# Kernel optimization log

Hardware: AMD Instinct MI355X
Metric: run time of the kernel (lower is better)

## Reference

```python
import jax, jax.numpy as jnp
import numpy as np

B, S, IN_DIM, LATENT, SYM = 16, 256, 512, 512, 128
NUM_NODES, NUM_CODES, MAX_OPS, MAX_BUS = 4, 512, 4, 32
HALT_EPS, MAX_SEQ = 1e-3, 256


def setup_inputs() -> dict:
    key = jax.random.key(0)
    ks = jax.random.split(key, 10)

    def lin(k, out_d, in_d, pre=()):
        kw, kb = jax.random.split(k)
        lim = 1.0 / np.sqrt(in_d).astype(np.float32)
        w = jax.random.uniform(kw, pre + (out_d, in_d), minval=-lim, maxval=lim, dtype=jnp.float32)
        b = jax.random.uniform(kb, pre + (out_d,), minval=-lim, maxval=lim, dtype=jnp.float32)
        return w, b

    x = jax.random.normal(ks[0], (B, S, IN_DIM), jnp.float32)
    ipw, ipb = lin(ks[1], LATENT, IN_DIM)
    tp = jax.random.normal(ks[2], (1, MAX_SEQ, LATENT), jnp.float32)
    N = (NUM_NODES,)
    sw, sb = lin(ks[3], SYM, LATENT, N)
    qw, qb = lin(ks[4], 1, SYM, N)
    rw, rb = lin(ks[5], LATENT, 2 * LATENT, N)
    c1w, c1b = lin(ks[6], LATENT, LATENT + SYM, N)
    c2w, c2b = lin(ks[7], LATENT, LATENT, N)
    cb = jax.random.normal(ks[8], (NUM_NODES, NUM_CODES, SYM), jnp.float32)
    return {"x": x, "input_proj_w": ipw, "input_proj_b": ipb, "token_prompts": tp,
            "sym_w": sw, "sym_b": sb, "qry_w": qw, "qry_b": qb,
            "read_w": rw, "read_b": rb, "c1_w": c1w, "c1_b": c1b,
            "c2_w": c2w, "c2_b": c2b, "codebook": cb}


def _forward(x, input_proj_w, input_proj_b, token_prompts, sym_w, sym_b, qry_w, qry_b,
             read_w, read_b, c1_w, c1_b, c2_w, c2_b, codebook):
    Bx, Sx, _ = x.shape
    N = Bx * Sx
    # input projection + positional prompts
    out = jnp.einsum('bsi,li->bsl', x, input_proj_w) + input_proj_b + token_prompts[:, :Sx, :]
    prev_out = out
    active = jnp.ones((Bx, Sx), bool)
    token_tags = jnp.zeros((Bx, Sx, SYM), x.dtype)
    # TensorBus rolling buffers ([max_bus, B, S, dim]); with default cfg the roll branch never fires
    sym_buf = jnp.zeros((MAX_BUS, Bx, Sx, SYM), x.dtype)          # slot 0 = zero tags (initial append)
    out_buf = jnp.zeros((MAX_BUS, Bx, Sx, LATENT), x.dtype).at[0].set(out)
    msg_mask = jnp.zeros((MAX_BUS,), bool).at[0].set(True)
    ptr = 1  # static python int: appends are a fixed unrolled schedule (1 + MAX_OPS*NUM_NODES <= MAX_BUS)
    slot_ids = jnp.arange(MAX_BUS)

    for t in range(MAX_OPS):
        # snapshot of active messages for this op step (get_active)
        snap_active = msg_mask & (slot_ids < ptr)                  # [MAX_BUS]
        syms_flat = sym_buf.reshape(MAX_BUS, N, SYM)
        outs_flat = out_buf.reshape(MAX_BUS, N, LATENT)
        keep_all = jnp.ones((MAX_BUS,), bool)
        for n in range(NUM_NODES):
            # relevance of each bus message per token; inactive slots masked out of argmax
            rel = jnp.einsum('tnd,d->tn', syms_flat, qry_w[n, 0]) + qry_b[n, 0]
            rel = jnp.where(snap_active[:, None], rel, jnp.asarray(-1e9, rel.dtype))
            top = jnp.argmax(rel, axis=0)                          # [N] chosen message per token
            chosen = jnp.take_along_axis(outs_flat, top[None, :, None], axis=0)[0]  # [N, LATENT]
            bus_ctx = chosen.reshape(Bx, Sx, LATENT)
            z = jnp.concatenate([out, bus_ctx], axis=-1)
            z_read = jnp.einsum('bsk,lk->bsl', z, read_w[n]) + read_b[n]
            raw_sym = jnp.einsum('bsl,dl->bsd', z_read, sym_w[n]) + sym_b[n]
            # EMA quantizer (eval): nearest codebook entry by euclidean distance
            flat = raw_sym.reshape(-1, SYM)
            cbn = codebook[n]
            d2 = (jnp.sum(flat * flat, axis=-1, keepdims=True)
                  - 2.0 * flat @ cbn.T + jnp.sum(cbn * cbn, axis=-1))
            idx = jnp.argmin(d2, axis=-1)
            quant = cbn[idx].reshape(Bx, Sx, SYM)
            h = jnp.concatenate([z_read, quant], axis=-1)
            hid = jax.nn.relu(jnp.einsum('bsk,lk->bsl', h, c1_w[n]) + c1_b[n])
            node_out = jnp.einsum('bsl,ol->bso', hid, c2_w[n]) + c2_b[n] + out
            # halting / selective update
            delta = jnp.linalg.norm(node_out - prev_out, axis=-1)
            halt = (delta < HALT_EPS) & active
            assigned = active if t > 0 else jnp.ones_like(active)
            upd = assigned & jnp.logical_not(halt)
            out = jnp.where(upd[..., None], node_out, out)
            token_tags = jnp.where(upd[..., None], quant, token_tags)
            # bus.append
            sym_buf = sym_buf.at[ptr].set(quant)
            out_buf = out_buf.at[ptr].set(node_out)
            msg_mask = msg_mask.at[ptr].set(True)
            ptr += 1
            # keep_mask: messages never selected by any token stay alive
            counts = jnp.zeros((MAX_BUS,), jnp.int32).at[top].add(1)
            keep_all = keep_all & (counts == 0)
            active = active & jnp.logical_not(halt)
            prev_out = out
        # mark_consumed: ones over valid slots ANDed with per-node keep masks at snapshot-active
        # slots (inactive/new slots get True -> faithful to the torch init_global_mask quirk)
        msg_mask = (slot_ids < ptr) & keep_all
    return out


def reference(x, input_proj_w, input_proj_b, token_prompts, sym_w, sym_b, qry_w, qry_b,
              read_w, read_b, c1_w, c1_b, c2_w, c2_b, codebook):
    return _forward(x, input_proj_w, input_proj_b, token_prompts, sym_w, sym_b, qry_w, qry_b,
                    read_w, read_b, c1_w, c1_b, c2_w, c2_b, codebook)
```

## Files before the change

kernel.cpp:

```cpp
#include <hip/hip_runtime.h>
#include <math.h>

namespace {

typedef _Float16 f16;
typedef __attribute__((ext_vector_type(8))) _Float16 f16x8;
typedef __attribute__((ext_vector_type(4))) float f32x4;

constexpr int TOK = 4096;
constexpr int DL  = 512;
constexpr int DS  = 128;
constexpr int NC  = 512;
constexpr int NSLOT = 13;

__device__ __forceinline__ float wsum(float v){
  #pragma unroll
  for(int o=32;o>0;o>>=1) v += __shfl_xor(v,o);
  return v;
}

__device__ __forceinline__ void gload16(const void* g, void* l){
  __builtin_amdgcn_global_load_lds(
      (const __attribute__((address_space(1))) unsigned int*)g,
      (__attribute__((address_space(3))) unsigned int*)l, 16, 0, 0);
}

__device__ __forceinline__ int slotb(int row, int g){
  return (((row ^ ((row>>2)&1))<<2) | (g ^ (row&3))) << 4;
}

template<int AMODE,int EPI>
__global__ __launch_bounds__(256,2) void mgemm(
    const f16* __restrict__ A1h, const f16* __restrict__ A1l,
    const f16* __restrict__ A2h, const f16* __restrict__ A2l,
    const int* __restrict__ gidx,
    const f16* __restrict__ Bh, const f16* __restrict__ Bl,
    const float* __restrict__ bias, const float* __restrict__ res,
    float* __restrict__ Cf, f16* __restrict__ Ch, f16* __restrict__ Cl,
    f16* __restrict__ C2h, f16* __restrict__ C2l,
    float* __restrict__ scpv, int* __restrict__ scpi, int* __restrict__ idxg,
    int K, int K0)
{
  constexpr int SMB = 16384;
  __shared__ __align__(16) char smem[3*SMB];
  __shared__ int gsel[64];
  __shared__ float redv[4][32];
  __shared__ int   redi[4][32];
  const int tid = threadIdx.x, w = tid>>6, l = tid&63;
  const int m0 = blockIdx.x*64, n0 = blockIdx.y*64;
  const int NK = K>>5, SW = K0>>5;

  if(AMODE==2){
    if(tid<64){
      int m = m0+tid;
      float bv = -INFINITY; int bi = 0;
      #pragma unroll
      for(int y=0;y<8;y++){
        float v = scpv[(size_t)y*TOK + m];
        if(v > bv){ bv=v; bi=scpi[(size_t)y*TOK + m]; }
      }
      gsel[tid]=bi;
      idxg[m]=bi;
    }
    __syncthreads();
  }

  const f16* sp[4]; const f16* sp2[4]; int loff[4];
  #pragma unroll
  for(int i=0;i<4;i++){
    int c = 4*w+i;
    int isA = (c<8);
    int plane = isA ? (c>>2) : ((c-8)>>2);
    int cidx  = isA ? (c&3)  : ((c-8)&3);
    loff[i] = (isA?0:8192) + plane*4096 + cidx*1024;
    int s = (cidx<<6) + l;
    int rp = s>>2, row = rp ^ ((rp>>2)&1), g = (s&3) ^ (row&3);
    int g8 = g<<3;
    if(isA){
      int m = m0 + row;
      const f16* p1 = (plane? A1l : A1h) + ((size_t)m<<9) + g8;
      sp[i] = p1;
      if(AMODE==1)      sp2[i] = (plane? A2l : A2h) + ((size_t)gidx[m]<<21) + ((size_t)m<<9) + g8;
      else if(AMODE==2) sp2[i] = (plane? A2l : A2h) + ((size_t)gsel[row]<<7) + g8;
      else              sp2[i] = p1;
    } else {
      sp[i] = (plane? Bl : Bh) + (size_t)(n0+row)*K + g8;
      sp2[i] = sp[i];
    }
  }

  const int wr = w>>1, wc = w&1, q = l>>4, r = l&15;
  int aoff[2], boff[2];
  #pragma unroll
  for(int i=0;i<2;i++) aoff[i] = slotb(32*wr + 16*i + r, q);
  #pragma unroll
  for(int j=0;j<2;j++) boff[j] = 8192 + slotb(32*wc + 16*j + r, q);

  f32x4 acc1[2][2] = {}, acc2[2][2] = {};

  auto advance = [&](int snext){
    #pragma unroll
    for(int i=0;i<4;i++){
      if(AMODE!=0 && (4*w+i)<8 && snext==SW) sp[i] = sp2[i];
      else                                    sp[i] += 32;
    }
  };

  #pragma unroll
  for(int i=0;i<4;i++) gload16(sp[i], smem + loff[i]);
  advance(1);
  #pragma unroll
  for(int i=0;i<4;i++) gload16(sp[i], smem + SMB + loff[i]);
  advance(2);
  asm volatile("s_waitcnt vmcnt(4)" ::: "memory");
  __builtin_amdgcn_s_barrier();

  int roff = 0, soff = 2*SMB;
  for(int kt=0; kt<NK; ++kt){
    const char* Lb = smem + roff;
    f16x8 ah[2], al[2], bh[2], bl[2];
    #pragma unroll
    for(int i=0;i<2;i++){
      ah[i] = *(const f16x8*)(Lb + aoff[i]);
      al[i] = *(const f16x8*)(Lb + 4096 + aoff[i]);
    }
    #pragma unroll
    for(int j=0;j<2;j++){
      bh[j] = *(const f16x8*)(Lb + boff[j]);
      bl[j] = *(const f16x8*)(Lb + 4096 + boff[j]);
    }
    if(kt+2 < NK){
      #pragma unroll
      for(int i=0;i<4;i++) gload16(sp[i], smem + soff + loff[i]);
      advance(kt+3);
    }
    #pragma unroll
    for(int i=0;i<2;i++)
      #pragma unroll
      for(int j=0;j<2;j++){
        acc1[i][j] = __builtin_amdgcn_mfma_f32_16x16x32_f16(ah[i], bh[j], acc1[i][j], 0,0,0);
        acc2[i][j] = __builtin_amdgcn_mfma_f32_16x16x32_f16(ah[i], bl[j], acc2[i][j], 0,0,0);
        acc2[i][j] = __builtin_amdgcn_mfma_f32_16x16x32_f16(al[i], bh[j], acc2[i][j], 0,0,0);
      }
    if(kt+2 < NK){
      asm volatile("s_waitcnt vmcnt(4)" ::: "memory");
      __builtin_amdgcn_s_barrier();
    } else if(kt+1 < NK){
      asm volatile("s_waitcnt vmcnt(0)" ::: "memory");
      __builtin_amdgcn_s_barrier();
    }
    roff = (roff==2*SMB)? 0 : roff+SMB;
    soff = (soff==2*SMB)? 0 : soff+SMB;
  }

  if(EPI!=1){
    #pragma unroll
    for(int i=0;i<2;i++)
      #pragma unroll
      for(int j=0;j<2;j++)
        #pragma unroll
        for(int rr=0;rr<4;rr++){
          int rowm = m0 + 32*wr + 16*i + 4*q + rr;
          int coln = n0 + 32*wc + 16*j + r;
          size_t o = ((size_t)rowm<<9) + coln;
          float v = acc1[i][j][rr] + acc2[i][j][rr]*(1.0f/2048.0f) + bias[coln];
          if(EPI==2) v = fmaxf(v, 0.f);
          if(EPI==3) v += res[o];
          if(EPI==4) v += res[(((size_t)(rowm&255))<<9) + coln];
          if(EPI==3 || EPI==4) Cf[o] = v;
          if(EPI==0 || EPI==2 || EPI==4){
            f16 h = (f16)v;
            Ch[o] = h; Cl[o] = (f16)((v-(float)h)*2048.0f);
          }
          if(EPI==4){
            f16 h = (f16)v;
            C2h[o] = h; C2l[o] = (f16)((v-(float)h)*2048.0f);
          }
        }
  } else {
    #pragma unroll
    for(int i=0;i<2;i++)
      #pragma unroll
      for(int rr=0;rr<4;rr++){
        float v0 = acc1[i][0][rr] + acc2[i][0][rr]*(1.0f/2048.0f) + bias[n0+32*wc+r];
        float v1 = acc1[i][1][rr] + acc2[i][1][rr]*(1.0f/2048.0f) + bias[n0+32*wc+16+r];
        float bv; int bc;
        if(v1 > v0){ bv=v1; bc=n0+32*wc+16+r; } else { bv=v0; bc=n0+32*wc+r; }
        #pragma unroll
        for(int o=1;o<16;o<<=1){
          float ov = __shfl_xor(bv,o); int oi = __shfl_xor(bc,o);
          if(ov>bv || (ov==bv && oi<bc)){ bv=ov; bc=oi; }
        }
        if(r==0){ redv[w][16*i+4*q+rr]=bv; redi[w][16*i+4*q+rr]=bc; }
      }
    __syncthreads();
    if(tid<64){
      int wr2 = tid>>5, li = tid&31;
      float bv = redv[2*wr2][li]; int bc = redi[2*wr2][li];
      float ov = redv[2*wr2+1][li]; int oi = redi[2*wr2+1][li];
      if(ov>bv || (ov==bv && oi<bc)){ bv=ov; bc=oi; }
      scpv[(size_t)blockIdx.y*TOK + m0 + tid] = bv;
      scpi[(size_t)blockIdx.y*TOK + m0 + tid] = bc;
    }
  }
}

__global__ void split_k(const float* __restrict__ src, f16* __restrict__ hi,
                        f16* __restrict__ lo, int n){
  for(int i = blockIdx.x*256 + threadIdx.x; i < n; i += gridDim.x*256){
    float v = src[i];
    f16 h = (f16)v;
    hi[i] = h;
    lo[i] = (f16)((v - (float)h)*2048.0f);
  }
}

__global__ __launch_bounds__(256)
void wcomb_k(const float* __restrict__ A, const float* __restrict__ Wall,
             float* __restrict__ C)
{
  constexpr int T=256;
  __shared__ float As[32][68];
  __shared__ float Ws[32][132];
  const int tid = threadIdx.x;
  const int m0 = blockIdx.x*64, n0 = blockIdx.y*128;
  const float* W = Wall + (size_t)(m0>>9)*DS*DL;
  const int ty = tid>>4, tx = tid&15;
  float4 pa[2], pw[4];
  auto loadA = [&](int k0){
    #pragma unroll
    for(int it=0; it<2; ++it){
      int v = tid + T*it; int rr = v>>3, c4 = v&7;
      pa[it] = *(const float4*)(A + (size_t)(m0+rr)*DS + k0 + (c4<<2));
    }
  };
  auto loadW = [&](int k0){
    #pragma unroll
    for(int it=0; it<4; ++it){
      int v = tid + T*it; int rr = v>>5, c4 = v&31;
      pw[it] = *(const float4*)(W + (size_t)(k0+rr)*DL + n0 + (c4<<2));
    }
  };
  float acc[4][8];
  #pragma unroll
  for(int i=0;i<4;i++)
    #pragma unroll
    for(int j=0;j<8;j++) acc[i][j]=0.f;
  loadA(0); loadW(0);
  for(int k0=0; k0<DS; k0+=32){
    __syncthreads();
    #pragma unroll
    for(int it=0; it<2; ++it){
      int v = tid + T*it; int rr=v>>3, c4=v&7;
      As[(c4<<2)+0][rr]=pa[it].x; As[(c4<<2)+1][rr]=pa[it].y;
      As[(c4<<2)+2][rr]=pa[it].z; As[(c4<<2)+3][rr]=pa[it].w;
    }
    #pragma unroll
    for(int it=0; it<4; ++it){
      int v = tid + T*it; int rr=v>>5, c4=v&31;
      *(float4*)&Ws[rr][c4<<2] = pw[it];
    }
    __syncthreads();
    if(k0+32 < DS){ loadA(k0+32); loadW(k0+32); }
    #pragma unroll
    for(int kk=0; kk<32; kk++){
      float4 a4 = *(const float4*)&As[kk][ty<<2];
      float4 b0 = *(const float4*)&Ws[kk][tx<<2];
      float4 b1 = *(const float4*)&Ws[kk][64+(tx<<2)];
      float a[4]={a4.x,a4.y,a4.z,a4.w};
      float b[8]={b0.x,b0.y,b0.z,b0.w,b1.x,b1.y,b1.z,b1.w};
      #pragma unroll
      for(int i=0;i<4;i++)
        #pragma unroll
        for(int j=0;j<8;j++) acc[i][j] = fmaf(a[i], b[j], acc[i][j]);
    }
  }
  #pragma unroll
  for(int i=0;i<4;i++){
    int m = m0 + (ty<<2) + i;
    #pragma unroll
    for(int j=0;j<8;j++){
      int n = n0 + ((j<4)? (tx<<2)+j : 64+(tx<<2)+(j-4));
      C[((size_t)m<<9)+n] = acc[i][j];
    }
  }
}

__global__ void init_k(int* __restrict__ msg, int* __restrict__ act,
                       float* __restrict__ relc, const float* __restrict__ qb,
                       int* __restrict__ cons){
  int i = blockIdx.x*256 + threadIdx.x;
  if(i < TOK){
    act[i] = 1;
    #pragma unroll
    for(int nn=0;nn<4;nn++) relc[nn*TOK + i] = qb[nn];
  }
  if(i < 32){ msg[i] = (i==0) ? 1 : 0; cons[i] = 0; }
}

__global__ void bias2_k(const float* __restrict__ cb, const float* __restrict__ sb,
                        float* __restrict__ b2){
  int row = blockIdx.x*4 + (threadIdx.x>>6);
  int lane = threadIdx.x&63;
  const float* cv = cb + ((size_t)row<<7);
  const float* sbn = sb + ((row>>9)<<7);
  float c0=cv[lane], c1=cv[lane+64];
  float nrm = c0*c0 + c1*c1;
  float dt  = c0*sbn[lane] + c1*sbn[lane+64];
  nrm = wsum(nrm); dt = wsum(dt);
  if(lane==0) b2[row] = dt - 0.5f*nrm;
}

__global__ void relmax_k(const float* __restrict__ relc, const int* __restrict__ msg,
                         int pt, int node, int* __restrict__ top, int* __restrict__ cons){
  int tok = blockIdx.x*256 + threadIdx.x;
  float best = -1e9f; int bs = 0;
  for(int s=0;s<pt;s++){
    float v = msg[s] ? relc[(size_t)((s<<2)+node)*TOK + tok] : -1e9f;
    if(v > best){ best = v; bs = s; }
  }
  top[tok] = bs;
  cons[bs] = 1;
}

__global__ void mupdate_k(const float* __restrict__ no_, float* __restrict__ out,
                          f16* __restrict__ outh, f16* __restrict__ outl,
                          f16* __restrict__ slabh, f16* __restrict__ slabl,
                          float* __restrict__ relc, const int* __restrict__ idx,
                          const float* __restrict__ cbn, const float* __restrict__ qw,
                          const float* __restrict__ qb, int* __restrict__ act,
                          int* __restrict__ cons, int* __restrict__ msg,
                          int t, int ptr, int pe){
  int m = blockIdx.x*4 + (threadIdx.x>>6);
  int lane = threadIdx.x&63;
  const float* nrow = no_ + ((size_t)m<<9);
  float* orow = out + ((size_t)m<<9);
  float nv[8]; float s=0.f;
  #pragma unroll
  for(int rr=0;rr<8;rr++){
    int c = lane + (rr<<6);
    nv[rr]=nrow[c];
    float d = nv[rr]-orow[c]; s += d*d;
  }
  s = wsum(s);
  float delta = sqrtf(s);
  int a = act[m];
  int halt = (delta < 1e-3f) && a;
  int assigned = (t>0) ? a : 1;
  int upd = assigned && !halt;
  if(lane==0) act[m] = a && !halt;
  if(upd){
    #pragma unroll
    for(int rr=0;rr<8;rr++){
      int c = lane + (rr<<6);
      float v = nv[rr];
      orow[c] = v;
      f16 h = (f16)v;
      outh[((size_t)m<<9)+c] = h;
      outl[((size_t)m<<9)+c] = (f16)((v-(float)h)*2048.0f);
    }
  }
  if(ptr >= 0){
    size_t so = (((size_t)ptr)<<21) + ((size_t)m<<9);
    #pragma unroll
    for(int rr=0;rr<8;rr++){
      int c = lane + (rr<<6);
      float v = nv[rr];
      f16 h = (f16)v;
      slabh[so+c] = h;
      slabl[so+c] = (f16)((v-(float)h)*2048.0f);
    }
    const float* qv = cbn + ((size_t)idx[m]<<7);
    float q0=qv[lane], q1=qv[lane+64];
    #pragma unroll
    for(int nn=0;nn<4;nn++){
      float pr = q0*qw[(nn<<7)+lane] + q1*qw[(nn<<7)+64+lane];
      pr = wsum(pr);
      if(lane==0) relc[(size_t)((ptr<<2)+nn)*TOK + m] = pr + qb[nn];
    }
  }
  if(pe >= 0 && blockIdx.x==0 && threadIdx.x < 32){
    int s2 = threadIdx.x;
    msg[s2] = (s2 < pe) && !cons[s2];
    cons[s2] = 0;
  }
}

}

extern "C" void kernel_launch(void* const* d_in, const int* in_sizes, int n_in,
                              void* d_out, int out_size, void* d_ws, size_t ws_size,
                              hipStream_t stream)
{
  (void)in_sizes; (void)n_in; (void)out_size; (void)ws_size;
  const float* x   = (const float*)d_in[0];
  const float* ipw = (const float*)d_in[1];
  const float* ipb = (const float*)d_in[2];
  const float* tp  = (const float*)d_in[3];
  const float* sw  = (const float*)d_in[4];
  const float* sb  = (const float*)d_in[5];
  const float* qw  = (const float*)d_in[6];
  const float* qb  = (const float*)d_in[7];
  const float* rw  = (const float*)d_in[8];
  const float* rb  = (const float*)d_in[9];
  const float* c1w = (const float*)d_in[10];
  const float* c1b = (const float*)d_in[11];
  const float* c2w = (const float*)d_in[12];
  const float* c2b = (const float*)d_in[13];
  const float* cb  = (const float*)d_in[14];
  float* out = (float*)d_out;

  char* p = (char*)d_ws;
  auto alloc = [&](size_t b)->char*{ char* r=p; p += (b+255)&~(size_t)255; return r; };
  f16* slabh = (f16*)alloc((size_t)NSLOT*TOK*DL*2);
  f16* slabl = (f16*)alloc((size_t)NSLOT*TOK*DL*2);
  f16* outh  = (f16*)alloc((size_t)TOK*DL*2);
  f16* outl  = (f16*)alloc((size_t)TOK*DL*2);
  f16* zh    = (f16*)alloc((size_t)TOK*DL*2);
  f16* zl    = (f16*)alloc((size_t)TOK*DL*2);
  f16* hh    = (f16*)alloc((size_t)TOK*DL*2);
  f16* hl    = (f16*)alloc((size_t)TOK*DL*2);
  float* sn  = (float*)alloc((size_t)TOK*DL*4);
  f16* rwh   = (f16*)alloc((size_t)4*DL*1024*2);
  f16* rwl   = (f16*)alloc((size_t)4*DL*1024*2);
  f16* c1h   = (f16*)alloc((size_t)4*DL*640*2);
  f16* c1l   = (f16*)alloc((size_t)4*DL*640*2);
  f16* c2h   = (f16*)alloc((size_t)4*DL*DL*2);
  f16* c2l   = (f16*)alloc((size_t)4*DL*DL*2);
  f16* wch   = (f16*)alloc((size_t)4*NC*DL*2);
  f16* wcl   = (f16*)alloc((size_t)4*NC*DL*2);
  f16* iph   = (f16*)alloc((size_t)DL*DL*2);
  f16* ipl   = (f16*)alloc((size_t)DL*DL*2);
  f16* cbh   = (f16*)alloc((size_t)4*NC*DS*2);
  f16* cbl   = (f16*)alloc((size_t)4*NC*DS*2);
  float* b2  = (float*)alloc(4*NC*4);
  float* relc= (float*)alloc((size_t)NSLOT*4*TOK*4);
  float* scpv= (float*)alloc((size_t)8*TOK*4);
  int* scpi  = (int*)alloc((size_t)8*TOK*4);
  int* top   = (int*)alloc(TOK*4);
  int* idxb  = (int*)alloc(TOK*4);
  int* act   = (int*)alloc(TOK*4);
  int* msg   = (int*)alloc(256);
  int* cons  = (int*)alloc(256);

  dim3 G(64,8), B(256);

  init_k<<<16,256,0,stream>>>(msg, act, relc, qb, cons);
  bias2_k<<<512,256,0,stream>>>(cb, sb, b2);
  wcomb_k<<<dim3(32,4),B,0,stream>>>(cb, sw, sn);
  split_k<<<2048,256,0,stream>>>(x,   hh,  hl,  TOK*DL);
  split_k<<<512 ,256,0,stream>>>(ipw, iph, ipl, DL*DL);
  split_k<<<2048,256,0,stream>>>(rw,  rwh, rwl, 4*DL*1024);
  split_k<<<2048,256,0,stream>>>(c1w, c1h, c1l, 4*DL*640);
  split_k<<<1024,256,0,stream>>>(c2w, c2h, c2l, 4*DL*DL);
  split_k<<<512 ,256,0,stream>>>(cb,  cbh, cbl, 4*NC*DS);
  split_k<<<1024,256,0,stream>>>(sn,  wch, wcl, 4*NC*DL);

  mgemm<0,4><<<G,B,0,stream>>>(hh,hl, nullptr,nullptr, nullptr, iph,ipl,
      ipb, tp, out, outh,outl, slabh,slabl, nullptr,nullptr,nullptr, DL, DL);

  int ptr = 1;
  for(int t=0;t<4;t++){
    int pt = 1 + 4*t;
    for(int n=0;n<4;n++){
      relmax_k<<<16,256,0,stream>>>(relc, msg, pt, n, top, cons);
      mgemm<1,0><<<G,B,0,stream>>>(outh,outl, slabh,slabl, top,
          rwh+(size_t)n*DL*1024, rwl+(size_t)n*DL*1024, rb+(size_t)n*DL,
          nullptr, nullptr, zh,zl, nullptr,nullptr, nullptr,nullptr,nullptr, 1024, 512);
      mgemm<0,1><<<G,B,0,stream>>>(zh,zl, nullptr,nullptr, nullptr,
          wch+(size_t)n*NC*DL, wcl+(size_t)n*NC*DL, b2+(size_t)n*NC,
          nullptr, nullptr, nullptr,nullptr, nullptr,nullptr, scpv,scpi,nullptr, 512, 512);
      mgemm<2,2><<<G,B,0,stream>>>(zh,zl, cbh+(size_t)n*NC*DS, cbl+(size_t)n*NC*DS, nullptr,
          c1h+(size_t)n*DL*640, c1l+(size_t)n*DL*640, c1b+(size_t)n*DL,
          nullptr, nullptr, hh,hl, nullptr,nullptr, scpv,scpi,idxb, 640, 512);
      mgemm<0,3><<<G,B,0,stream>>>(hh,hl, nullptr,nullptr, nullptr,
          c2h+(size_t)n*DL*DL, c2l+(size_t)n*DL*DL, c2b+(size_t)n*DL,
          out, sn, nullptr,nullptr, nullptr,nullptr, nullptr,nullptr,nullptr, 512, 512);
      mupdate_k<<<1024,256,0,stream>>>(sn, out, outh,outl, slabh,slabl, relc, idxb,
          cb+(size_t)n*NC*DS, qw, qb, act, cons, msg, t,
          (t<3)? ptr : -1, (n==3 && t<3)? (1+4*(t+1)) : -1);
      ptr++;
    }
  }
}
```

Baseline: 1.305 ms.

## Enlarge GEMM M-tile to 128, fuse relmax and slab split into GEMMs, batch splits

The GEMM tile grows from 64x64 to 128x64. Each wave now computes 4x2 MFMA fragments, which needs larger LDS buffers and half as many blocks. The relmax kernel is folded into the prologue of the read GEMM, the hi/lo slab write moves from mupdate into the c2 GEMM epilogue, and five weight split launches are merged into one. Together these cut launches and redundant global traffic. The cost is lower occupancy and grid parallelism (256 blocks), and the per-tile relmax loop is now recomputed in every column block.

```diff
diff --git a/kernel.cpp b/kernel.cpp
--- a/kernel.cpp
+++ b/kernel.cpp
@@ -33,25 +33,39 @@
 __global__ __launch_bounds__(256,2) void mgemm(
     const f16* __restrict__ A1h, const f16* __restrict__ A1l,
     const f16* __restrict__ A2h, const f16* __restrict__ A2l,
-    const int* __restrict__ gidx,
     const f16* __restrict__ Bh, const f16* __restrict__ Bl,
     const float* __restrict__ bias, const float* __restrict__ res,
     float* __restrict__ Cf, f16* __restrict__ Ch, f16* __restrict__ Cl,
     f16* __restrict__ C2h, f16* __restrict__ C2l,
     float* __restrict__ scpv, int* __restrict__ scpi, int* __restrict__ idxg,
+    const float* __restrict__ relc, const int* __restrict__ msg,
+    int* __restrict__ cons, int pt, int node,
     int K, int K0)
 {
-  constexpr int SMB = 16384;
+  constexpr int SMB = 24576;
   __shared__ __align__(16) char smem[3*SMB];
-  __shared__ int gsel[64];
-  __shared__ float redv[4][32];
-  __shared__ int   redi[4][32];
+  __shared__ int gsel[128];
+  __shared__ float redv[4][64];
+  __shared__ int   redi[4][64];
   const int tid = threadIdx.x, w = tid>>6, l = tid&63;
-  const int m0 = blockIdx.x*64, n0 = blockIdx.y*64;
+  const int m0 = blockIdx.x*128, n0 = blockIdx.y*64;
   const int NK = K>>5, SW = K0>>5;
 
+  if(AMODE==1){
+    if(tid<128){
+      int m = m0+tid;
+      float best = -1e9f; int bs = 0;
+      for(int s=0;s<pt;s++){
+        float v = msg[s] ? relc[(size_t)((s<<2)+node)*TOK + m] : -1e9f;
+        if(v > best){ best=v; bs=s; }
+      }
+      gsel[tid]=bs;
+      cons[bs]=1;
+    }
+    __syncthreads();
+  }
   if(AMODE==2){
-    if(tid<64){
+    if(tid<128){
       int m = m0+tid;
       float bv = -INFINITY; int bi = 0;
       #pragma unroll
@@ -65,14 +79,14 @@
     __syncthreads();
   }
 
-  const f16* sp[4]; const f16* sp2[4]; int loff[4];
-  #pragma unroll
-  for(int i=0;i<4;i++){
-    int c = 4*w+i;
-    int isA = (c<8);
-    int plane = isA ? (c>>2) : ((c-8)>>2);
-    int cidx  = isA ? (c&3)  : ((c-8)&3);
-    loff[i] = (isA?0:8192) + plane*4096 + cidx*1024;
+  const f16* sp[6]; const f16* sp2[6]; int loff[6];
+  #pragma unroll
+  for(int i=0;i<6;i++){
+    int c = 6*w+i;
+    int isA = (c<16);
+    int plane = isA ? (c>>3) : ((c-16)>>2);
+    int cidx  = isA ? (c&7)  : ((c-16)&3);
+    loff[i] = isA ? (plane*8192 + cidx*1024) : (16384 + plane*4096 + cidx*1024);
     int s = (cidx<<6) + l;
     int rp = s>>2, row = rp ^ ((rp>>2)&1), g = (s&3) ^ (row&3);
     int g8 = g<<3;
@@ -80,7 +94,7 @@
       int m = m0 + row;
       const f16* p1 = (plane? A1l : A1h) + ((size_t)m<<9) + g8;
       sp[i] = p1;
-      if(AMODE==1)      sp2[i] = (plane? A2l : A2h) + ((size_t)gidx[m]<<21) + ((size_t)m<<9) + g8;
+      if(AMODE==1)      sp2[i] = (plane? A2l : A2h) + ((size_t)gsel[row]<<21) + ((size_t)m<<9) + g8;
       else if(AMODE==2) sp2[i] = (plane? A2l : A2h) + ((size_t)gsel[row]<<7) + g8;
       else              sp2[i] = p1;
     } else {
@@ -90,39 +104,39 @@
   }
 
   const int wr = w>>1, wc = w&1, q = l>>4, r = l&15;
-  int aoff[2], boff[2];
-  #pragma unroll
-  for(int i=0;i<2;i++) aoff[i] = slotb(32*wr + 16*i + r, q);
-  #pragma unroll
-  for(int j=0;j<2;j++) boff[j] = 8192 + slotb(32*wc + 16*j + r, q);
-
-  f32x4 acc1[2][2] = {}, acc2[2][2] = {};
+  int aoff[4], boff[2];
+  #pragma unroll
+  for(int i=0;i<4;i++) aoff[i] = slotb(64*wr + 16*i + r, q);
+  #pragma unroll
+  for(int j=0;j<2;j++) boff[j] = 16384 + slotb(32*wc + 16*j + r, q);
+
+  f32x4 acc1[4][2] = {}, acc2[4][2] = {};
 
   auto advance = [&](int snext){
     #pragma unroll
-    for(int i=0;i<4;i++){
-      if(AMODE!=0 && (4*w+i)<8 && snext==SW) sp[i] = sp2[i];
-      else                                    sp[i] += 32;
+    for(int i=0;i<6;i++){
+      if(AMODE!=0 && (6*w+i)<16 && snext==SW) sp[i] = sp2[i];
+      else                                     sp[i] += 32;
     }
   };
 
   #pragma unroll
-  for(int i=0;i<4;i++) gload16(sp[i], smem + loff[i]);
+  for(int i=0;i<6;i++) gload16(sp[i], smem + loff[i]);
   advance(1);
   #pragma unroll
-  for(int i=0;i<4;i++) gload16(sp[i], smem + SMB + loff[i]);
+  for(int i=0;i<6;i++) gload16(sp[i], smem + SMB + loff[i]);
   advance(2);
-  asm volatile("s_waitcnt vmcnt(4)" ::: "memory");
+  asm volatile("s_waitcnt vmcnt(6)" ::: "memory");
   __builtin_amdgcn_s_barrier();
 
   int roff = 0, soff = 2*SMB;
   for(int kt=0; kt<NK; ++kt){
     const char* Lb = smem + roff;
-    f16x8 ah[2], al[2], bh[2], bl[2];
-    #pragma unroll
-    for(int i=0;i<2;i++){
+    f16x8 ah[4], al[4], bh[2], bl[2];
+    #pragma unroll
+    for(int i=0;i<4;i++){
       ah[i] = *(const f16x8*)(Lb + aoff[i]);
-      al[i] = *(const f16x8*)(Lb + 4096 + aoff[i]);
+      al[i] = *(const f16x8*)(Lb + 8192 + aoff[i]);
     }
     #pragma unroll
     for(int j=0;j<2;j++){
@@ -131,11 +145,11 @@
     }
     if(kt+2 < NK){
       #pragma unroll
-      for(int i=0;i<4;i++) gload16(sp[i], smem + soff + loff[i]);
+      for(int i=0;i<6;i++) gload16(sp[i], smem + soff + loff[i]);
       advance(kt+3);
     }
     #pragma unroll
-    for(int i=0;i<2;i++)
+    for(int i=0;i<4;i++)
       #pragma unroll
       for(int j=0;j<2;j++){
         acc1[i][j] = __builtin_amdgcn_mfma_f32_16x16x32_f16(ah[i], bh[j], acc1[i][j], 0,0,0);
@@ -143,7 +157,7 @@
         acc2[i][j] = __builtin_amdgcn_mfma_f32_16x16x32_f16(al[i], bh[j], acc2[i][j], 0,0,0);
       }
     if(kt+2 < NK){
-      asm volatile("s_waitcnt vmcnt(4)" ::: "memory");
+      asm volatile("s_waitcnt vmcnt(6)" ::: "memory");
       __builtin_amdgcn_s_barrier();
     } else if(kt+1 < NK){
       asm volatile("s_waitcnt vmcnt(0)" ::: "memory");
@@ -155,12 +169,12 @@
 
   if(EPI!=1){
     #pragma unroll
-    for(int i=0;i<2;i++)
+    for(int i=0;i<4;i++)
       #pragma unroll
       for(int j=0;j<2;j++)
         #pragma unroll
         for(int rr=0;rr<4;rr++){
-          int rowm = m0 + 32*wr + 16*i + 4*q + rr;
+          int rowm = m0 + 64*wr + 16*i + 4*q + rr;
           int coln = n0 + 32*wc + 16*j + r;
           size_t o = ((size_t)rowm<<9) + coln;
           float v = acc1[i][j][rr] + acc2[i][j][rr]*(1.0f/2048.0f) + bias[coln];
@@ -172,14 +186,14 @@
             f16 h = (f16)v;
             Ch[o] = h; Cl[o] = (f16)((v-(float)h)*2048.0f);
           }
-          if(EPI==4){
+          if((EPI==3 || EPI==4) && C2h){
             f16 h = (f16)v;
             C2h[o] = h; C2l[o] = (f16)((v-(float)h)*2048.0f);
           }
         }
   } else {
     #pragma unroll
-    for(int i=0;i<2;i++)
+    for(int i=0;i<4;i++)
       #pragma unroll
       for(int rr=0;rr<4;rr++){
         float v0 = acc1[i][0][rr] + acc2[i][0][rr]*(1.0f/2048.0f) + bias[n0+32*wc+r];
@@ -194,10 +208,10 @@
         if(r==0){ redv[w][16*i+4*q+rr]=bv; redi[w][16*i+4*q+rr]=bc; }
       }
     __syncthreads();
-    if(tid<64){
-      int wr2 = tid>>5, li = tid&31;
-      float bv = redv[2*wr2][li]; int bc = redi[2*wr2][li];
-      float ov = redv[2*wr2+1][li]; int oi = redi[2*wr2+1][li];
+    if(tid<128){
+      int wrs = tid>>6, li = tid&63;
+      float bv = redv[2*wrs][li]; int bc = redi[2*wrs][li];
+      float ov = redv[2*wrs+1][li]; int oi = redi[2*wrs+1][li];
       if(ov>bv || (ov==bv && oi<bc)){ bv=ov; bc=oi; }
       scpv[(size_t)blockIdx.y*TOK + m0 + tid] = bv;
       scpi[(size_t)blockIdx.y*TOK + m0 + tid] = bc;
@@ -212,6 +226,23 @@
     f16 h = (f16)v;
     hi[i] = h;
     lo[i] = (f16)((v - (float)h)*2048.0f);
+  }
+}
+
+struct SplitArg { const float* src; f16* hi; f16* lo; int n; };
+struct SplitArgs5 { SplitArg a[5]; };
+__global__ void splitm_k(SplitArgs5 A){
+  int stride = gridDim.x*256;
+  #pragma unroll
+  for(int s=0;s<5;s++){
+    const float* src = A.a[s].src; f16* hi = A.a[s].hi; f16* lo = A.a[s].lo;
+    int n = A.a[s].n;
+    for(int i = blockIdx.x*256 + threadIdx.x; i < n; i += stride){
+      float v = src[i];
+      f16 h = (f16)v;
+      hi[i] = h;
+      lo[i] = (f16)((v - (float)h)*2048.0f);
+    }
   }
 }
 
@@ -311,21 +342,8 @@
   if(lane==0) b2[row] = dt - 0.5f*nrm;
 }
 
-__global__ void relmax_k(const float* __restrict__ relc, const int* __restrict__ msg,
-                         int pt, int node, int* __restrict__ top, int* __restrict__ cons){
-  int tok = blockIdx.x*256 + threadIdx.x;
-  float best = -1e9f; int bs = 0;
-  for(int s=0;s<pt;s++){
-    float v = msg[s] ? relc[(size_t)((s<<2)+node)*TOK + tok] : -1e9f;
-    if(v > best){ best = v; bs = s; }
-  }
-  top[tok] = bs;
-  cons[bs] = 1;
-}
-
 __global__ void mupdate_k(const float* __restrict__ no_, float* __restrict__ out,
                           f16* __restrict__ outh, f16* __restrict__ outl,
-                          f16* __restrict__ slabh, f16* __restrict__ slabl,
                           float* __restrict__ relc, const int* __restrict__ idx,
                           const float* __restrict__ cbn, const float* __restrict__ qw,
                           const float* __restrict__ qb, int* __restrict__ act,
@@ -361,15 +379,6 @@
     }
   }
   if(ptr >= 0){
-    size_t so = (((size_t)ptr)<<21) + ((size_t)m<<9);
-    #pragma unroll
-    for(int rr=0;rr<8;rr++){
-      int c = lane + (rr<<6);
-      float v = nv[rr];
-      f16 h = (f16)v;
-      slabh[so+c] = h;
-      slabl[so+c] = (f16)((v-(float)h)*2048.0f);
-    }
     const float* qv = cbn + ((size_t)idx[m]<<7);
     float q0=qv[lane], q1=qv[lane+64];
     #pragma unroll
@@ -437,46 +446,53 @@
   float* relc= (float*)alloc((size_t)NSLOT*4*TOK*4);
   float* scpv= (float*)alloc((size_t)8*TOK*4);
   int* scpi  = (int*)alloc((size_t)8*TOK*4);
-  int* top   = (int*)alloc(TOK*4);
   int* idxb  = (int*)alloc(TOK*4);
   int* act   = (int*)alloc(TOK*4);
   int* msg   = (int*)alloc(256);
   int* cons  = (int*)alloc(256);
 
-  dim3 G(64,8), B(256);
+  dim3 G(32,8), B(256);
 
   init_k<<<16,256,0,stream>>>(msg, act, relc, qb, cons);
   bias2_k<<<512,256,0,stream>>>(cb, sb, b2);
   wcomb_k<<<dim3(32,4),B,0,stream>>>(cb, sw, sn);
-  split_k<<<2048,256,0,stream>>>(x,   hh,  hl,  TOK*DL);
-  split_k<<<512 ,256,0,stream>>>(ipw, iph, ipl, DL*DL);
-  split_k<<<2048,256,0,stream>>>(rw,  rwh, rwl, 4*DL*1024);
-  split_k<<<2048,256,0,stream>>>(c1w, c1h, c1l, 4*DL*640);
-  split_k<<<1024,256,0,stream>>>(c2w, c2h, c2l, 4*DL*DL);
-  split_k<<<512 ,256,0,stream>>>(cb,  cbh, cbl, 4*NC*DS);
-  split_k<<<1024,256,0,stream>>>(sn,  wch, wcl, 4*NC*DL);
-
-  mgemm<0,4><<<G,B,0,stream>>>(hh,hl, nullptr,nullptr, nullptr, iph,ipl,
-      ipb, tp, out, outh,outl, slabh,slabl, nullptr,nullptr,nullptr, DL, DL);
+  split_k<<<2048,256,0,stream>>>(x, hh, hl, TOK*DL);
+  SplitArgs5 sa;
+  sa.a[0] = { ipw, iph, ipl, DL*DL };
+  sa.a[1] = { rw,  rwh, rwl, 4*DL*1024 };
+  sa.a[2] = { c1w, c1h, c1l, 4*DL*640 };
+  sa.a[3] = { c2w, c2h, c2l, 4*DL*DL };
+  sa.a[4] = { cb,  cbh, cbl, 4*NC*DS };
+  splitm_k<<<2048,256,0,stream>>>(sa);
+  split_k<<<1024,256,0,stream>>>(sn, wch, wcl, 4*NC*DL);
+
+  mgemm<0,4><<<G,B,0,stream>>>(hh,hl, nullptr,nullptr, iph,ipl,
+      ipb, tp, out, outh,outl, slabh,slabl,
+      nullptr,nullptr,nullptr, nullptr,nullptr,nullptr, 0,0, DL, DL);
 
   int ptr = 1;
   for(int t=0;t<4;t++){
     int pt = 1 + 4*t;
     for(int n=0;n<4;n++){
-      relmax_k<<<16,256,0,stream>>>(relc, msg, pt, n, top, cons);
-      mgemm<1,0><<<G,B,0,stream>>>(outh,outl, slabh,slabl, top,
+      mgemm<1,0><<<G,B,0,stream>>>(outh,outl, slabh,slabl,
           rwh+(size_t)n*DL*1024, rwl+(size_t)n*DL*1024, rb+(size_t)n*DL,
-          nullptr, nullptr, zh,zl, nullptr,nullptr, nullptr,nullptr,nullptr, 1024, 512);
-      mgemm<0,1><<<G,B,0,stream>>>(zh,zl, nullptr,nullptr, nullptr,
+          nullptr, nullptr, zh,zl, nullptr,nullptr,
+          nullptr,nullptr,nullptr, relc, msg, cons, pt, n, 1024, 512);
+      mgemm<0,1><<<G,B,0,stream>>>(zh,zl, nullptr,nullptr,
           wch+(size_t)n*NC*DL, wcl+(size_t)n*NC*DL, b2+(size_t)n*NC,
-          nullptr, nullptr, nullptr,nullptr, nullptr,nullptr, scpv,scpi,nullptr, 512, 512);
-      mgemm<2,2><<<G,B,0,stream>>>(zh,zl, cbh+(size_t)n*NC*DS, cbl+(size_t)n*NC*DS, nullptr,
+          nullptr, nullptr, nullptr,nullptr, nullptr,nullptr,
+          scpv,scpi,nullptr, nullptr,nullptr,nullptr, 0,0, 512, 512);
+      mgemm<2,2><<<G,B,0,stream>>>(zh,zl, cbh+(size_t)n*NC*DS, cbl+(size_t)n*NC*DS,
           c1h+(size_t)n*DL*640, c1l+(size_t)n*DL*640, c1b+(size_t)n*DL,
-          nullptr, nullptr, hh,hl, nullptr,nullptr, scpv,scpi,idxb, 640, 512);
-      mgemm<0,3><<<G,B,0,stream>>>(hh,hl, nullptr,nullptr, nullptr,
+          nullptr, nullptr, hh,hl, nullptr,nullptr,
+          scpv,scpi,idxb, nullptr,nullptr,nullptr, 0,0, 640, 512);
+      f16* sph = (t<3) ? slabh + ((size_t)ptr<<21) : nullptr;
+      f16* spl = (t<3) ? slabl + ((size_t)ptr<<21) : nullptr;
+      mgemm<0,3><<<G,B,0,stream>>>(hh,hl, nullptr,nullptr,
           c2h+(size_t)n*DL*DL, c2l+(size_t)n*DL*DL, c2b+(size_t)n*DL,
-          out, sn, nullptr,nullptr, nullptr,nullptr, nullptr,nullptr,nullptr, 512, 512);
-      mupdate_k<<<1024,256,0,stream>>>(sn, out, outh,outl, slabh,slabl, relc, idxb,
+          out, sn, nullptr,nullptr, sph,spl,
+          nullptr,nullptr,nullptr, nullptr,nullptr,nullptr, 0,0, 512, 512);
+      mupdate_k<<<1024,256,0,stream>>>(sn, out, outh,outl, relc, idxb,
           cb+(size_t)n*NC*DS, qw, qb, act, cons, msg, t,
           (t<3)? ptr : -1, (n==3 && t<3)? (1+4*(t+1)) : -1);
       ptr++;
```

After: 1.522 ms. +16.6%, slower.
